# Performance work log

Hardware: AMD Instinct MI355X
Metric: run time of the kernel (lower is better)

The kernel has to match this reference:

```python
import jax, jax.numpy as jnp
import numpy as np

B, ORG, L = 128, 4, 2048
C1, C2 = 128, 64
K0, K1, K2 = 7, 5, 3
VQD, VQN = 64, 1024
CARD, NG = 32, 8
EPS = 1e-5


def _conv(x, w, groups=1):
    # 1D conv, stride 1, 'same' padding (k-1)//2, NCH layout, weight (O, I/g, K)
    p = (w.shape[-1] - 1) // 2
    return jax.lax.conv_general_dilated(
        x, w, (1,), [(p, p)],
        dimension_numbers=('NCH', 'OIH', 'NCH'), feature_group_count=groups)


def _tconv(x, w):
    # ConvTranspose1d(stride=1, padding=(k-1)//2) == conv with channel-transposed, spatially flipped kernel
    return _conv(x, jnp.flip(jnp.transpose(w, (1, 0, 2)), -1))


def _gn(x, g, b, groups=NG):
    Bx, C, T = x.shape
    xr = x.reshape(Bx, groups, C // groups, T)
    mu = xr.mean((2, 3), keepdims=True)
    var = xr.var((2, 3), keepdims=True)
    xn = ((xr - mu) * jax.lax.rsqrt(var + EPS)).reshape(Bx, C, T)
    return xn * g[None, :, None] + b[None, :, None]


def setup_inputs() -> dict:
    key = jax.random.key(0)
    ks = iter(jax.random.split(key, 32))
    w = lambda *s: jax.random.normal(next(ks), s, jnp.float32) * 0.05
    ones = lambda n: jnp.ones((n,), jnp.float32)
    zeros = lambda n: jnp.zeros((n,), jnp.float32)
    D = C1 // 2  # ResNeXt bottleneck width
    return dict(
        x=jax.random.normal(next(ks), (B, ORG, L), jnp.float32),
        w0=w(C1, ORG, K0), g0_g=ones(C1), g0_b=zeros(C1),
        wxa=w(D, C1, 1), gxa_g=ones(D), gxa_b=zeros(D),
        wxb=w(D, D // CARD, K1), gxb_g=ones(D), gxb_b=zeros(D),
        wxc=w(C1, D, 1), gxc_g=ones(C1), gxc_b=zeros(C1),
        w2=w(C2, C1, K2), bn2_g=ones(C2), bn2_b=zeros(C2),
        embed_w=jax.random.uniform(next(ks), (VQN, VQD), jnp.float32, -1.0 / VQD, 1.0 / VQD),
        wd2=w(C2, C1, K2), gd2_g=ones(C1), gd2_b=zeros(C1),
        wd1a=w(C1, C1, K1), gd1a_g=ones(C1), gd1a_b=zeros(C1),
        wd1b=w(C1, C1, K1), gd1b_g=ones(C1), gd1b_b=zeros(C1),
        wd0=w(C1, ORG, K0), bd0=zeros(ORG),
    )


def reference(x, w0, g0_g, g0_b, wxa, gxa_g, gxa_b, wxb, gxb_g, gxb_b,
              wxc, gxc_g, gxc_b, w2, bn2_g, bn2_b, embed_w,
              wd2, gd2_g, gd2_b, wd1a, gd1a_g, gd1a_b, wd1b, gd1b_g, gd1b_b,
              wd0, bd0):
    selu = jax.nn.selu

    # ---- encoder ----
    h = selu(_gn(_conv(x, w0), g0_g, g0_b))  # res0

    def resx(h):  # ResNeXt bottleneck, shared weights (module reuses self.resx)
        y = selu(_gn(_conv(h, wxa), gxa_g, gxa_b))
        y = selu(_gn(_conv(y, wxb, groups=CARD), gxb_g, gxb_b))
        y = _gn(_conv(y, wxc), gxc_g, gxc_b)
        return selu(h + y)

    pool = lambda t: t.reshape(t.shape[0], t.shape[1], -1, 2).max(-1)  # MaxPool1d(2)
    h = pool(resx(h))
    h = pool(resx(h))
    # res2: conv + BatchNorm (eval mode, running stats 0/1 -> affine)
    h = _conv(h, w2) * bn2_g[None, :, None] + bn2_b[None, :, None]

    # ---- vector quantization (vqc=True: quantize channel vectors) ----
    Bh, C, T = h.shape  # C == VQD
    Z = jnp.transpose(h, (0, 2, 1)).reshape(-1, VQD)  # [N, vq_dim]
    d = (jnp.sum(Z * Z, 1, keepdims=True) - 2.0 * (Z @ embed_w.T)
         + jnp.sum(embed_w * embed_w, 1)[None, :])  # [N, vq_num] squared L2
    j = jnp.argmin(d, axis=1)
    W_j = embed_w[j]
    commit_loss = jnp.mean(jnp.sum((Z - jax.lax.stop_gradient(W_j)) ** 2, -1))
    vq_loss = jnp.mean(jnp.sum((jax.lax.stop_gradient(Z) - W_j) ** 2, -1))
    hq = jnp.transpose(W_j.reshape(Bh, T, C), (0, 2, 1))  # back to [B, C, T]

    # ---- decoder ----
    up = lambda t: jnp.repeat(t, 2, axis=-1)  # nearest Upsample(x2)

    def deres1(h):  # basic residual block, shared weights (module reuses self.deres1)
        y = selu(_gn(_tconv(h, wd1a), gd1a_g, gd1a_b))
        y = _gn(_tconv(y, wd1b), gd1b_g, gd1b_b)
        return selu(h + y)

    h = selu(_gn(_tconv(hq, wd2), gd2_g, gd2_b))  # deres2
    h = deres1(up(h))
    h = deres1(up(h))
    recon = _tconv(h, wd0) + bd0[None, :, None]  # deres0 (with bias)
    return recon, commit_loss, vq_loss
```

## Files before the change

kernel.cpp:

```cpp
#include <hip/hip_runtime.h>
#include <math.h>

static constexpr int B_   = 128;
static constexpr int ORG_ = 4;
static constexpr int L_   = 2048;
static constexpr int C1_  = 128;
static constexpr int C2_  = 64;
static constexpr int NG_  = 8;
static constexpr int VQD_ = 64;
static constexpr int VQN_ = 1024;
static constexpr long PTS_ = (long)B_ * (L_ / 4);

typedef __attribute__((ext_vector_type(8))) short bf16x8;
typedef __attribute__((ext_vector_type(4))) float f32x4;

__device__ __forceinline__ float selu_f(float x) {
    const float scale = 1.0507009873554805f;
    const float alpha = 1.6732632423543772f;
    return scale * (x > 0.f ? x : alpha * expm1f(x));
}
__device__ __forceinline__ unsigned short f2bf(float x) {
    unsigned u = __float_as_uint(x);
    u = (u + 0x7FFFu + ((u >> 16) & 1u)) >> 16;
    return (unsigned short)u;
}
__device__ __forceinline__ float bf2f(unsigned short u) {
    return __uint_as_float((unsigned)u << 16);
}

__global__ void wprep_kernel(const float* __restrict__ w, float* __restrict__ wT,
                             int CO, int cig, int K, int so, int si, int sk, int koff)
{
    int idx = blockIdx.x * 256 + threadIdx.x;
    int total = cig * K * CO;
    if (idx >= total) return;
    int o = idx % CO;
    int r = idx / CO;
    int i = r / K, k = r % K;
    wT[idx] = w[(long)o * so + (long)i * si + (long)k * sk + koff];
}

__global__ void wprep_mfma_kernel(const float* __restrict__ w, unsigned short* __restrict__ wb)
{
    int idx = blockIdx.x * 256 + threadIdx.x;
    if (idx >= 5 * 16 * 128 * 8) return;
    int j  = idx & 7;
    int o  = (idx >> 3) & 127;
    int kk = idx >> 10;
    int ig = kk & 3, ic = (kk >> 2) & 3, k = kk >> 4;
    int i  = ic * 32 + ig * 8 + j;
    wb[idx] = f2bf(w[(long)i * (128 * 5) + o * 5 + (4 - k)]);
}

__global__ void fill_kernel(float* p, float v, int n)
{
    int i = blockIdx.x * 256 + threadIdx.x;
    if (i < n) p[i] = v;
}

template<int K, int CO, int NTHR, int TT, int OT, int VQ>
__global__ __launch_bounds__(NTHR) void conv_tile_kernel(
    const float* __restrict__ in, const float* __restrict__ wT,
    const float* __restrict__ scale, const float* __restrict__ bias,
    float* __restrict__ out,
    int CI, int T, int cig, int cog,
    const float* __restrict__ ist, const float* __restrict__ ig,
    const float* __restrict__ ibt, int icpg, int iselu,
    const float* __restrict__ res,
    float* __restrict__ vbest, int* __restrict__ vbj, int jbase, long vstride)
{
    constexpr int P    = (K - 1) / 2;
    constexpr int SPAN = TT + K - 1;
    constexpr int RS   = (SPAN + 3) & ~3;
    constexpr int NO   = CO / OT;
    constexpr int NT   = (CO * TT) / (NTHR * OT);
    constexpr int XW   = NT + K - 1;
    extern __shared__ float lds[];

    if constexpr (VQ) {
        const int z = blockIdx.z;
        wT    += (long)z * cig * K * CO;
        bias  += (long)z * CO;
        vbest += (long)z * vstride;
        vbj   += (long)z * vstride;
        jbase += z * CO;
    }

    const int tile = blockIdx.x;
    const int b    = blockIdx.y;
    const int t0g  = tile * TT;
    const float* inb = in + (long)b * CI * T;

    for (int idx = threadIdx.x; idx < CI * SPAN; idx += NTHR) {
        int c = idx / SPAN, j = idx % SPAN;
        int tt = t0g + j - P;
        float v = 0.f;
        if (tt >= 0 && tt < T) {
            v = inb[(long)c * T + tt];
            if (ist) {
                const float* s = &ist[2 * (b * NG_ + c / icpg)];
                v = (v - s[0]) * s[1] * ig[c] + ibt[c];
                if (res) v += res[((long)b * CI + c) * T + tt];
                if (iselu) v = selu_f(v);
            }
        }
        lds[c * RS + j] = v;
    }
    __syncthreads();

    const int o0   = (threadIdx.x % NO) * OT;
    const int slot = threadIdx.x / NO;
    const int t0   = slot * NT;
    const int g    = o0 / cog;
    const float* wrow = wT + o0;

    float acc[OT][NT];
#pragma unroll
    for (int oo = 0; oo < OT; ++oo)
#pragma unroll
        for (int u = 0; u < NT; ++u) acc[oo][u] = 0.f;

#pragma unroll 4
    for (int i = 0; i < cig; ++i) {
        const int irow = g * cig + i;
        float xin[(XW + 3) & ~3];
        if constexpr (NT % 4 == 0) {
            constexpr int X4 = (XW + 3) / 4;
            const float4* l4 = reinterpret_cast<const float4*>(&lds[irow * RS + t0]);
#pragma unroll
            for (int j = 0; j < X4; ++j) {
                float4 v = l4[j];
                xin[4 * j]     = v.x;
                xin[4 * j + 1] = v.y;
                xin[4 * j + 2] = v.z;
                xin[4 * j + 3] = v.w;
            }
        } else {
#pragma unroll
            for (int j = 0; j < XW; ++j) xin[j] = lds[irow * RS + t0 + j];
        }
        float wk[OT][K];
#pragma unroll
        for (int oo = 0; oo < OT; ++oo)
#pragma unroll
            for (int k = 0; k < K; ++k) wk[oo][k] = wrow[(i * K + k) * CO + oo];
#pragma unroll
        for (int oo = 0; oo < OT; ++oo)
#pragma unroll
            for (int u = 0; u < NT; ++u)
#pragma unroll
                for (int k = 0; k < K; ++k)
                    acc[oo][u] = fmaf(xin[u + k], wk[oo][k], acc[oo][u]);
    }

    if constexpr (VQ) {
        constexpr int RW = (NO >= 64) ? 64 : 32;
        const int lane = threadIdx.x & 63;
#pragma unroll
        for (int u = 0; u < NT; ++u) {
            float bv = 3.4e38f;
            int bj = 0;
#pragma unroll
            for (int oo = 0; oo < OT; ++oo) {
                const int o = o0 + oo;
                float sv = fmaf(acc[oo][u], scale[o], bias[o]);
                if (sv < bv) { bv = sv; bj = jbase + o; }
            }
#pragma unroll
            for (int off = 1; off < RW; off <<= 1) {
                float v2 = __shfl_xor(bv, off);
                int   j2 = __shfl_xor(bj, off);
                if (v2 < bv || (v2 == bv && j2 < bj)) { bv = v2; bj = j2; }
            }
            if ((lane & (RW - 1)) == 0) {
                long n = (long)b * T + t0g + t0 + u;
                vbest[n] = bv;
                vbj[n]   = bj;
            }
        }
    } else {
#pragma unroll
        for (int oo = 0; oo < OT; ++oo) {
            const int o = o0 + oo;
            const float sc = scale ? scale[o] : 1.f;
            const float bi = bias  ? bias[o]  : 0.f;
            float* ob = out + ((long)b * CO + o) * T + t0g + t0;
#pragma unroll
            for (int u = 0; u < NT; ++u) ob[u] = acc[oo][u] * sc + bi;
        }
    }
}

__global__ __launch_bounds__(256) void conv_epi7_kernel(
    const unsigned short* __restrict__ in, const float* __restrict__ wT,
    float* __restrict__ pbuf, int T, int Bc,
    const float* __restrict__ ist, const float* __restrict__ ig_,
    const float* __restrict__ ibt, int icpg,
    const unsigned short* __restrict__ res)
{
    __shared__ float wlds[32 * 7 * 4];
    __shared__ float rows[4][80];

    const int z   = blockIdx.z;
    const int ci0 = z * 32;

    for (int idx = threadIdx.x; idx < 32 * 7 * 4; idx += 256)
        wlds[idx] = wT[ci0 * 7 * 4 + idx];
    __syncthreads();

    const int wid  = threadIdx.x >> 6;
    const int lane = threadIdx.x & 63;
    const int b    = blockIdx.y;
    const int t0w  = blockIdx.x * 256 + wid * 64;
    const int t    = t0w + lane;
    float* row = rows[wid];
    const long base = (long)b * 128 * T;

    float acc0 = 0.f, acc1 = 0.f, acc2 = 0.f, acc3 = 0.f;

    for (int cc = 0; cc < 32; ++cc) {
        const int ci = ci0 + cc;
        const float* s = &ist[2 * (b * NG_ + ci / icpg)];
        const float mu = s[0], rs = s[1];
        const float gc = ig_[ci], bc = ibt[ci];
        const long cbase = base + (long)ci * T;

        float v = bf2f(in[cbase + t]);
        v = (v - mu) * rs * gc + bc;
        v += bf2f(res[cbase + t]);
        v = selu_f(v);
        row[3 + lane] = v;

        if (lane < 3 || lane >= 61) {
            int th   = (lane < 3) ? (t0w - 3 + lane) : (t0w + 3 + lane);
            int ridx = (lane < 3) ? lane : (lane + 6);
            float h = 0.f;
            if (th >= 0 && th < T) {
                h = bf2f(in[cbase + th]);
                h = (h - mu) * rs * gc + bc;
                h += bf2f(res[cbase + th]);
                h = selu_f(h);
            }
            row[ridx] = h;
        }

        float xin[7];
#pragma unroll
        for (int j = 0; j < 7; ++j) xin[j] = row[lane + j];
#pragma unroll
        for (int k = 0; k < 7; ++k) {
            float4 w4 = *(const float4*)&wlds[(cc * 7 + k) * 4];
            acc0 = fmaf(xin[k], w4.x, acc0);
            acc1 = fmaf(xin[k], w4.y, acc1);
            acc2 = fmaf(xin[k], w4.z, acc2);
            acc3 = fmaf(xin[k], w4.w, acc3);
        }
    }

    const long half = (long)Bc * 4 * T;
    float* pb = pbuf + (long)z * half + ((long)b * 4) * T + t;
    pb[0 * T] = acc0;
    pb[1 * T] = acc1;
    pb[2 * T] = acc2;
    pb[3 * T] = acc3;
}

__global__ void epi_comb_kernel(const float* __restrict__ pbuf,
                                const float* __restrict__ bias,
                                float* __restrict__ out, int T, int Bc, long total)
{
    const long half = (long)Bc * 4 * T;
    for (long idx = blockIdx.x * (long)blockDim.x + threadIdx.x; idx < total;
         idx += (long)gridDim.x * blockDim.x) {
        const int o = (int)((idx / T) & 3);
        float v = ((pbuf[idx] + pbuf[half + idx]) + pbuf[2 * half + idx])
                  + pbuf[3 * half + idx];
        out[idx] = v + bias[o];
    }
}

__global__ __launch_bounds__(256) void conv_mfma5_kernel(
    const unsigned short* __restrict__ in, const unsigned short* __restrict__ wb,
    unsigned short* __restrict__ out, int T,
    const float* __restrict__ ist, const float* __restrict__ ig_,
    const float* __restrict__ ibt, int icpg)
{
    constexpr int SPAN = 68, RSI = 136;
    __shared__ unsigned short xlds[SPAN * RSI];

    const int t0g = blockIdx.x * 64;
    const int b   = blockIdx.y;
    const unsigned short* inb = in + (long)b * 128 * T;

    for (int idx = threadIdx.x; idx < 128 * SPAN; idx += 256) {
        int i = idx / SPAN, j = idx % SPAN;
        int tt = t0g + j - 2;
        unsigned short raw = 0;
        if (tt >= 0 && tt < T) {
            raw = inb[(long)i * T + tt];
            if (ist) {
                const float* s = &ist[2 * (b * NG_ + i / icpg)];
                float v = selu_f((bf2f(raw) - s[0]) * s[1] * ig_[i] + ibt[i]);
                raw = f2bf(v);
            }
        }
        xlds[j * RSI + i] = raw;
    }
    __syncthreads();

    const int lane = threadIdx.x & 63;
    const int wid  = threadIdx.x >> 6;
    const int mr   = lane & 15;
    const int kg   = lane >> 4;

    f32x4 acc[4][2];
#pragma unroll
    for (int m = 0; m < 4; ++m)
#pragma unroll
        for (int oo = 0; oo < 2; ++oo) acc[m][oo] = (f32x4){0.f, 0.f, 0.f, 0.f};

#pragma unroll
    for (int k = 0; k < 5; ++k) {
#pragma unroll
        for (int ic = 0; ic < 4; ++ic) {
            bf16x8 a[4];
#pragma unroll
            for (int m = 0; m < 4; ++m)
                a[m] = *(const bf16x8*)&xlds[(m * 16 + mr + k) * RSI + ic * 32 + kg * 8];
            const unsigned short* wp = wb + (((k * 16 + ic * 4 + kg) * 128) + mr) * 8;
#pragma unroll
            for (int oo = 0; oo < 2; ++oo) {
                const int ot = wid * 2 + oo;
                bf16x8 bfr = *(const bf16x8*)(wp + ot * 16 * 8);
#pragma unroll
                for (int m = 0; m < 4; ++m)
                    acc[m][oo] = __builtin_amdgcn_mfma_f32_16x16x32_bf16(a[m], bfr, acc[m][oo], 0, 0, 0);
            }
        }
    }

#pragma unroll
    for (int m = 0; m < 4; ++m) {
#pragma unroll
        for (int oo = 0; oo < 2; ++oo) {
            const int ot = wid * 2 + oo;
            int o = ot * 16 + mr;
            ushort4 v;
            v.x = f2bf(acc[m][oo][0]);
            v.y = f2bf(acc[m][oo][1]);
            v.z = f2bf(acc[m][oo][2]);
            v.w = f2bf(acc[m][oo][3]);
            *(ushort4*)&out[((long)b * 128 + o) * T + t0g + m * 16 + kg * 4] = v;
        }
    }
}

__global__ __launch_bounds__(256) void gn_stats_kernel(
    const float* __restrict__ x, float* __restrict__ stats,
    int C, int T, int G)
{
    const int bg = blockIdx.x;
    const int cpg = C / G;
    const int b = bg / G, g = bg % G;
    const float* base = x + ((long)b * C + (long)g * cpg) * T;
    const long n4 = (long)cpg * T / 4;
    const float4* b4 = (const float4*)base;
    float s = 0.f, ss = 0.f;
    for (long i = threadIdx.x; i < n4; i += blockDim.x) {
        float4 v = b4[i];
        s += v.x + v.y + v.z + v.w;
        ss += v.x * v.x + v.y * v.y + v.z * v.z + v.w * v.w;
    }
#pragma unroll
    for (int off = 32; off; off >>= 1) {
        s  += __shfl_down(s, off);
        ss += __shfl_down(ss, off);
    }
    __shared__ float sh_s[4], sh_ss[4];
    const int wid = threadIdx.x >> 6, lane = threadIdx.x & 63;
    if (lane == 0) { sh_s[wid] = s; sh_ss[wid] = ss; }
    __syncthreads();
    if (threadIdx.x == 0) {
        float S = 0.f, SS = 0.f;
        for (int i = 0; i < 4; ++i) { S += sh_s[i]; SS += sh_ss[i]; }
        float inv_n = 1.f / (float)((long)cpg * T);
        float mu  = S * inv_n;
        float var = SS * inv_n - mu * mu;
        stats[2 * bg]     = mu;
        stats[2 * bg + 1] = rsqrtf(var + 1e-5f);
    }
}

__global__ __launch_bounds__(256) void gn_stats_bf16_kernel(
    const unsigned short* __restrict__ x, float* __restrict__ stats,
    int C, int T, int G)
{
    const int bg = blockIdx.x;
    const int cpg = C / G;
    const int b = bg / G, g = bg % G;
    const unsigned short* base = x + ((long)b * C + (long)g * cpg) * T;
    const long n8 = (long)cpg * T / 8;
    const uint4* b8 = (const uint4*)base;
    float s = 0.f, ss = 0.f;
    for (long i = threadIdx.x; i < n8; i += blockDim.x) {
        uint4 v = b8[i];
        unsigned ws[4] = {v.x, v.y, v.z, v.w};
#pragma unroll
        for (int q = 0; q < 4; ++q) {
            float f0 = __uint_as_float(ws[q] << 16);
            float f1 = __uint_as_float(ws[q] & 0xFFFF0000u);
            s += f0 + f1;
            ss += f0 * f0 + f1 * f1;
        }
    }
#pragma unroll
    for (int off = 32; off; off >>= 1) {
        s  += __shfl_down(s, off);
        ss += __shfl_down(ss, off);
    }
    __shared__ float sh_s[4], sh_ss[4];
    const int wid = threadIdx.x >> 6, lane = threadIdx.x & 63;
    if (lane == 0) { sh_s[wid] = s; sh_ss[wid] = ss; }
    __syncthreads();
    if (threadIdx.x == 0) {
        float S = 0.f, SS = 0.f;
        for (int i = 0; i < 4; ++i) { S += sh_s[i]; SS += sh_ss[i]; }
        float inv_n = 1.f / (float)((long)cpg * T);
        float mu  = S * inv_n;
        float var = SS * inv_n - mu * mu;
        stats[2 * bg]     = mu;
        stats[2 * bg + 1] = rsqrtf(var + 1e-5f);
    }
}

__global__ __launch_bounds__(256) void pool_fused_kernel(
    const float* __restrict__ x, const float* __restrict__ xst,
    const float* __restrict__ xg, const float* __restrict__ xb, int xcpg,
    const float* __restrict__ r, const float* __restrict__ rst,
    const float* __restrict__ rg, const float* __restrict__ rb, int rcpg, int rselu,
    float* __restrict__ out, int C, int Tout, long total)
{
    for (long idx = blockIdx.x * (long)blockDim.x + threadIdx.x; idx < total;
         idx += (long)gridDim.x * blockDim.x) {
        const int to = (int)(idx % Tout);
        const int c  = (int)((idx / Tout) % C);
        const int b  = (int)(idx / ((long)Tout * C));
        const long base = ((long)b * C + c) * (2 * Tout);
        const float* sx = &xst[2 * (b * NG_ + c / xcpg)];
        const float xgc = sx[1] * xg[c], xbc = xb[c] - sx[0] * sx[1] * xg[c];
        float rgc = 1.f, rbc = 0.f;
        if (rst) {
            const float* sr = &rst[2 * (b * NG_ + c / rcpg)];
            rgc = sr[1] * rg[c]; rbc = rb[c] - sr[0] * sr[1] * rg[c];
        }
        float f[2];
#pragma unroll
        for (int q = 0; q < 2; ++q) {
            long t = base + 2 * to + q;
            float rv = r[t] * rgc + rbc;
            if (rst && rselu) rv = selu_f(rv);
            f[q] = selu_f(x[t] * xgc + xbc + rv);
        }
        out[((long)b * C + c) * Tout + to] = fmaxf(f[0], f[1]);
    }
}

template<int INBF>
__global__ __launch_bounds__(256) void up_fused_kernel(
    const void* __restrict__ x_, const float* __restrict__ xst,
    const float* __restrict__ xg, const float* __restrict__ xb, int xcpg,
    const unsigned short* __restrict__ res,
    unsigned short* __restrict__ out, int C, int Tin, long total)
{
    for (long idx = blockIdx.x * (long)blockDim.x + threadIdx.x; idx < total;
         idx += (long)gridDim.x * blockDim.x) {
        const int t = (int)(idx % Tin);
        const int c = (int)((idx / Tin) % C);
        const int b = (int)(idx / ((long)Tin * C));
        const float* s = &xst[2 * (b * NG_ + c / xcpg)];
        float v = INBF ? bf2f(((const unsigned short*)x_)[idx])
                       : ((const float*)x_)[idx];
        v = (v - s[0]) * s[1] * xg[c] + xb[c];
        if (res) v += bf2f(res[idx]);
        v = selu_f(v);
        unsigned short h = f2bf(v);
        unsigned pack = (unsigned)h | ((unsigned)h << 16);
        *(unsigned*)(out + (((long)b * C + c) * Tin + t) * 2) = pack;
    }
}

__global__ void wnorm_kernel(const float* __restrict__ codes, float* __restrict__ wn)
{
    int j = blockIdx.x * 256 + threadIdx.x;
    if (j >= VQN_) return;
    const float* c = codes + (long)j * VQD_;
    float s = 0.f;
#pragma unroll
    for (int i = 0; i < VQD_; ++i) s = fmaf(c[i], c[i], s);
    wn[j] = s;
}

__global__ void vq_combine_kernel(const float* __restrict__ vb, const int* __restrict__ vj,
                                  int* __restrict__ bjs, long stride, int NP)
{
    int n = blockIdx.x * 256 + threadIdx.x;
    if (n >= NP) return;
    float best = vb[n];
    int bj = vj[n];
#pragma unroll
    for (int s = 1; s < 4; ++s) {
        float v = vb[(long)s * stride + n];
        if (v < best) { best = v; bj = vj[(long)s * stride + n]; }
    }
    bjs[n] = bj;
}

__global__ __launch_bounds__(256) void vq_gather_kernel(
    const float* __restrict__ h, const float* __restrict__ codes,
    const int* __restrict__ bjs, float* __restrict__ hq, float* __restrict__ loss,
    int T)
{
    const int n0 = blockIdx.x * 64;
    const int b  = n0 / T;
    const int tb = n0 % T;
    __shared__ int sbj[64];
    if (threadIdx.x < 64) sbj[threadIdx.x] = bjs[n0 + threadIdx.x];
    __syncthreads();

    float l = 0.f;
#pragma unroll
    for (int r = 0; r < (VQD_ * 64) / 256; ++r) {
        int idx = r * 256 + (int)threadIdx.x;
        int c  = idx >> 6, tl = idx & 63;
        float wv = codes[(long)sbj[tl] * VQD_ + c];
        long off = ((long)b * VQD_ + c) * T + tb + tl;
        hq[off] = wv;
        float df = h[off] - wv;
        l = fmaf(df, df, l);
    }
#pragma unroll
    for (int off = 32; off; off >>= 1) l += __shfl_down(l, off);
    if ((threadIdx.x & 63) == 0) atomicAdd(loss, l);
}

__global__ void zero_kernel(float* p) { p[0] = 0.f; }

__global__ void finalize_kernel(const float* __restrict__ loss, float* __restrict__ out,
                                float invNP, long off)
{
    float v = loss[0] * invNP;
    out[off]     = v;
    out[off + 1] = v;
}

static inline int nblk(long total, int thr = 256, long cap = 262144) {
    long b = (total + thr - 1) / thr;
    if (b > cap) b = cap;
    if (b < 1) b = 1;
    return (int)b;
}
static inline int ldsz(int CI, int K, int TT = 64) {
    int span = TT + K - 1;
    int rs = (span + 3) & ~3;
    return CI * rs * 4;
}

struct WT {
    long w0, wxa, wxb, wxc, w2, wd2, wd0, total;
};
static WT wt_offsets() {
    WT o; long p = 0;
    o.w0   = p; p += (long)ORG_ * 7 * C1_;
    o.wxa  = p; p += (long)C1_ * 1 * (C1_ / 2);
    o.wxb  = p; p += 2L * 5 * (C1_ / 2);
    o.wxc  = p; p += (long)(C1_ / 2) * 1 * C1_;
    o.w2   = p; p += (long)C1_ * 3 * C2_;
    o.wd2  = p; p += (long)C2_ * 3 * C1_;
    o.wd0  = p; p += (long)C1_ * 7 * ORG_;
    o.total = p;
    return o;
}

static void run_chunk(const float* x, const float* const* W, const float* wt,
                      const WT& wo, const unsigned short* wbA, const unsigned short* wbB,
                      const float* wn, const float* wts, const float* neg2,
                      float* vbest4, int* vbj4, int* bjs, float* out,
                      float* A, float* Bb, float* Cc, float* st, float* lossbuf,
                      int Bc, long nbuf, hipStream_t stream)
{
    const float* g0_g  = W[1];
    const float* g0_b  = W[2];
    const float* gxa_g = W[4];
    const float* gxa_b = W[5];
    const float* gxb_g = W[7];
    const float* gxb_b = W[8];
    const float* gxc_g = W[10];
    const float* gxc_b = W[11];
    const float* bn2_g = W[13];
    const float* bn2_b = W[14];
    const float* embed = W[15];
    const float* gd2_g = W[17];
    const float* gd2_b = W[18];
    const float* gd1a_g= W[20];
    const float* gd1a_b= W[21];
    const float* gd1b_g= W[23];
    const float* gd1b_b= W[24];
    const float* bd0   = W[26];

    const int D_ = C1_ / 2;
    const int SLOT = 2048;
    float* st0 = st + 0 * SLOT;
    float* st1 = st + 1 * SLOT;
    float* st2 = st + 2 * SLOT;
    float* st3 = st + 3 * SLOT;
    float* st4 = st + 4 * SLOT;
    float* st5 = st + 5 * SLOT;
    float* st6 = st + 6 * SLOT;

    unsigned short* Au  = (unsigned short*)A;
    unsigned short* Bbu = (unsigned short*)Bb;
    unsigned short* Ccu = (unsigned short*)Cc;

    const int nbg = Bc * NG_;
    const int cpg1 = C1_ / NG_;

    int T = L_;

    conv_tile_kernel<7, 128, 512, 64, 1, 0><<<dim3(T / 64, Bc), 512, ldsz(ORG_, 7), stream>>>(
        x, wt + wo.w0, nullptr, nullptr, A, ORG_, T, ORG_, C1_,
        nullptr, nullptr, nullptr, 0, 0, nullptr, nullptr, nullptr, 0, 0);
    gn_stats_kernel<<<nbg, 256, 0, stream>>>(A, st0, C1_, T, NG_);

    conv_tile_kernel<1, 64, 512, 64, 2, 0><<<dim3(T / 64, Bc), 512, ldsz(C1_, 1), stream>>>(
        A, wt + wo.wxa, nullptr, nullptr, Bb, C1_, T, C1_, D_,
        st0, g0_g, g0_b, cpg1, 1, nullptr, nullptr, nullptr, 0, 0);
    gn_stats_kernel<<<nbg, 256, 0, stream>>>(Bb, st1, D_, T, NG_);

    conv_tile_kernel<5, 64, 512, 64, 1, 0><<<dim3(T / 64, Bc), 512, ldsz(D_, 5), stream>>>(
        Bb, wt + wo.wxb, nullptr, nullptr, Bb + nbuf / 2, D_, T, 2, 2,
        st1, gxa_g, gxa_b, D_ / NG_, 1, nullptr, nullptr, nullptr, 0, 0);
    gn_stats_kernel<<<nbg, 256, 0, stream>>>(Bb + nbuf / 2, st2, D_, T, NG_);

    conv_tile_kernel<1, 128, 512, 64, 2, 0><<<dim3(T / 64, Bc), 512, ldsz(D_, 1), stream>>>(
        Bb + nbuf / 2, wt + wo.wxc, nullptr, nullptr, Cc, D_, T, D_, C1_,
        st2, gxb_g, gxb_b, D_ / NG_, 1, nullptr, nullptr, nullptr, 0, 0);
    gn_stats_kernel<<<nbg, 256, 0, stream>>>(Cc, st3, C1_, T, NG_);

    {
        int Tout = T / 2;
        long tt = (long)Bc * C1_ * Tout;
        pool_fused_kernel<<<nblk(tt), 256, 0, stream>>>(
            Cc, st3, gxc_g, gxc_b, cpg1,
            A, st0, g0_g, g0_b, cpg1, 1,
            Bb, C1_, Tout, tt);
        T = Tout;
    }

    conv_tile_kernel<1, 64, 512, 64, 2, 0><<<dim3(T / 64, Bc), 512, ldsz(C1_, 1), stream>>>(
        Bb, wt + wo.wxa, nullptr, nullptr, Cc, C1_, T, C1_, D_,
        nullptr, nullptr, nullptr, 0, 0, nullptr, nullptr, nullptr, 0, 0);
    gn_stats_kernel<<<nbg, 256, 0, stream>>>(Cc, st1, D_, T, NG_);

    conv_tile_kernel<5, 64, 512, 64, 1, 0><<<dim3(T / 64, Bc), 512, ldsz(D_, 5), stream>>>(
        Cc, wt + wo.wxb, nullptr, nullptr, Cc + nbuf / 2, D_, T, 2, 2,
        st1, gxa_g, gxa_b, D_ / NG_, 1, nullptr, nullptr, nullptr, 0, 0);
    gn_stats_kernel<<<nbg, 256, 0, stream>>>(Cc + nbuf / 2, st2, D_, T, NG_);

    conv_tile_kernel<1, 128, 512, 64, 2, 0><<<dim3(T / 64, Bc), 512, ldsz(D_, 1), stream>>>(
        Cc + nbuf / 2, wt + wo.wxc, nullptr, nullptr, A, D_, T, D_, C1_,
        st2, gxb_g, gxb_b, D_ / NG_, 1, nullptr, nullptr, nullptr, 0, 0);
    gn_stats_kernel<<<nbg, 256, 0, stream>>>(A, st3, C1_, T, NG_);

    {
        int Tout = T / 2;
        long tt = (long)Bc * C1_ * Tout;
        pool_fused_kernel<<<nblk(tt), 256, 0, stream>>>(
            A, st3, gxc_g, gxc_b, cpg1,
            Bb, nullptr, nullptr, nullptr, 0, 0,
            Cc, C1_, Tout, tt);
        T = Tout;
    }

    conv_tile_kernel<3, 64, 512, 64, 1, 0><<<dim3(T / 64, Bc), 512, ldsz(C1_, 3), stream>>>(
        Cc, wt + wo.w2, bn2_g, bn2_b, Bb, C1_, T, C1_, C2_,
        nullptr, nullptr, nullptr, 0, 0, nullptr, nullptr, nullptr, 0, 0);

    {
        int NP = Bc * T;
        conv_tile_kernel<1, 256, 512, 64, 8, 1><<<dim3(T / 64, Bc, 4), 512,
                                                  ldsz(VQD_, 1), stream>>>(
            Bb, wts, neg2, wn, nullptr,
            VQD_, T, VQD_, 256,
            nullptr, nullptr, nullptr, 0, 0, nullptr,
            vbest4, vbj4, 0, PTS_);
        vq_combine_kernel<<<(NP + 255) / 256, 256, 0, stream>>>(vbest4, vbj4, bjs, PTS_, NP);
        vq_gather_kernel<<<NP / 64, 256, 0, stream>>>(Bb, embed, bjs, A, lossbuf, T);
    }

    conv_tile_kernel<3, 128, 512, 64, 1, 0><<<dim3(T / 64, Bc), 512, ldsz(C2_, 3), stream>>>(
        A, wt + wo.wd2, nullptr, nullptr, Bb, C2_, T, C2_, C1_,
        nullptr, nullptr, nullptr, 0, 0, nullptr, nullptr, nullptr, 0, 0);
    gn_stats_kernel<<<nbg, 256, 0, stream>>>(Bb, st4, C1_, T, NG_);

    {
        long tt = (long)Bc * C1_ * T;
        up_fused_kernel<0><<<nblk(tt), 256, 0, stream>>>(
            Bb, st4, gd2_g, gd2_b, cpg1, nullptr, Ccu, C1_, T, tt);
        T *= 2;
    }

    conv_mfma5_kernel<<<dim3(T / 64, Bc), 256, 0, stream>>>(
        Ccu, wbA, Au, T, nullptr, nullptr, nullptr, 0);
    gn_stats_bf16_kernel<<<nbg, 256, 0, stream>>>(Au, st5, C1_, T, NG_);

    conv_mfma5_kernel<<<dim3(T / 64, Bc), 256, 0, stream>>>(
        Au, wbB, Bbu, T, st5, gd1a_g, gd1a_b, cpg1);
    gn_stats_bf16_kernel<<<nbg, 256, 0, stream>>>(Bbu, st6, C1_, T, NG_);

    {
        long tt = (long)Bc * C1_ * T;
        up_fused_kernel<1><<<nblk(tt), 256, 0, stream>>>(
            Bbu, st6, gd1b_g, gd1b_b, cpg1, Ccu, Au, C1_, T, tt);
        T *= 2;
    }

    conv_mfma5_kernel<<<dim3(T / 64, Bc), 256, 0, stream>>>(
        Au, wbA, Ccu, T, nullptr, nullptr, nullptr, 0);
    gn_stats_bf16_kernel<<<nbg, 256, 0, stream>>>(Ccu, st5, C1_, T, NG_);

    conv_mfma5_kernel<<<dim3(T / 64, Bc), 256, 0, stream>>>(
        Ccu, wbB, Bbu, T, st5, gd1a_g, gd1a_b, cpg1);
    gn_stats_bf16_kernel<<<nbg, 256, 0, stream>>>(Bbu, st6, C1_, T, NG_);

    {
        float* pbuf = Cc;
        conv_epi7_kernel<<<dim3(T / 256, Bc, 4), 256, 0, stream>>>(
            Bbu, wt + wo.wd0, pbuf, T, Bc,
            st6, gd1b_g, gd1b_b, cpg1, Au);
        long tt = (long)Bc * 4 * T;
        epi_comb_kernel<<<nblk(tt), 256, 0, stream>>>(pbuf, bd0, out, T, Bc, tt);
    }
}

extern "C" void kernel_launch(void* const* d_in, const int* in_sizes, int n_in,
                              void* d_out, int out_size, void* d_ws, size_t ws_size,
                              hipStream_t stream) {
    const float* x = (const float*)d_in[0];
    const float* W[27];
    for (int i = 0; i < 27; ++i) W[i] = (const float*)d_in[i + 1];

    float* out = (float*)d_out;
    const WT wo = wt_offsets();

    const long WT_F32  = 262144;
    const long WB_F32  = 2 * 81920 / 2;
    const long WTS_F32 = VQN_ * VQD_;
    const long ST_F32  = 8 * 2048;
    const long VQ_F32  = 4 * PTS_ + 4 * PTS_ + PTS_;
    const long FIXED = WT_F32 + WB_F32 + 1024 + WTS_F32 + 256 + ST_F32 + 64 + VQ_F32;
    int Bc = 0;
    for (int cand = B_; cand >= 1; cand >>= 1) {
        size_t need = ((size_t)FIXED + (size_t)3 * cand * C1_ * L_) * sizeof(float);
        if (need <= ws_size) { Bc = cand; break; }
    }
    if (Bc == 0) return;

    float* wt            = (float*)d_ws;
    unsigned short* wbA  = (unsigned short*)(wt + WT_F32);
    unsigned short* wbB  = wbA + 81920;
    float* wn            = wt + WT_F32 + WB_F32;
    float* wts           = wn + 1024;
    float* neg2          = wts + WTS_F32;
    float* st            = neg2 + 256;
    float* lossbuf       = st + ST_F32;
    float* vbest4        = lossbuf + 64;
    int*   vbj4          = (int*)(vbest4 + 4 * PTS_);
    int*   bjs           = vbj4 + 4 * PTS_;
    const long nbuf = (long)Bc * C1_ * L_;
    float* A  = (float*)(bjs + PTS_);
    float* Bb = A + nbuf;
    float* Cc = Bb + nbuf;

    const int D_ = C1_ / 2;

    auto prep = [&](const float* w, long off, int CO, int cig, int K,
                    int so, int si, int sk, int koff) {
        int total = cig * K * CO;
        wprep_kernel<<<(total + 255) / 256, 256, 0, stream>>>(
            w, wt + off, CO, cig, K, so, si, sk, koff);
    };
    prep(W[0],  wo.w0,   C1_, ORG_, 7, ORG_ * 7, 7,        1,  0);
    prep(W[3],  wo.wxa,  D_,  C1_,  1, C1_,      1,        1,  0);
    prep(W[6],  wo.wxb,  D_,  2,    5, 2 * 5,    5,        1,  0);
    prep(W[9],  wo.wxc,  C1_, D_,   1, D_,       1,        1,  0);
    prep(W[12], wo.w2,   C2_, C1_,  3, C1_ * 3,  3,        1,  0);
    prep(W[16], wo.wd2,  C1_, C2_,  3, 3,        C1_ * 3, -1,  2);
    prep(W[25], wo.wd0,  ORG_, C1_, 7, 7,        ORG_ * 7, -1, 6);
    wprep_mfma_kernel<<<81920 / 256, 256, 0, stream>>>(W[19], wbA);
    wprep_mfma_kernel<<<81920 / 256, 256, 0, stream>>>(W[22], wbB);
    wnorm_kernel<<<(VQN_ + 255) / 256, 256, 0, stream>>>(W[15], wn);
    for (int q = 0; q < 4; ++q) {
        wprep_kernel<<<(256 * VQD_ + 255) / 256, 256, 0, stream>>>(
            W[15] + (long)q * 256 * VQD_, wts + (long)q * 256 * VQD_,
            256, VQD_, 1, VQD_, 1, 1, 0);
    }
    fill_kernel<<<1, 256, 0, stream>>>(neg2, -2.f, 256);

    zero_kernel<<<1, 1, 0, stream>>>(lossbuf);

    for (int b0 = 0; b0 < B_; b0 += Bc) {
        const float* xc = x + (long)b0 * ORG_ * L_;
        float* outc = out + (long)b0 * ORG_ * L_;
        run_chunk(xc, W, wt, wo, wbA, wbB, wn, wts, neg2, vbest4, vbj4, bjs,
                  outc, A, Bb, Cc, st, lossbuf, Bc, nbuf, stream);
    }

    {
        float invNP = 1.f / (float)(B_ * (L_ / 4));
        finalize_kernel<<<1, 1, 0, stream>>>(lossbuf, out, invNP, (long)out_size - 2);
    }
}
```

Baseline: 2.022 ms.

## Fuse GroupNorm statistics into the MFMA conv epilogue via atomics

The 5-tap bf16 MFMA conv kernel now reduces per-group sum and sum-of-squares from its fp32 accumulators. It adds them into a zeroed workspace buffer with atomicAdd, and a tiny finalize kernel turns them into mean and rstd. This replaces the four gn_stats_bf16 passes, which re-read the large upsampled decoder activations from memory. The trade-offs are atomic contention across time tiles, an extra zeroing launch, and stats taken from unrounded fp32 values instead of the stored bf16 output.

```diff
diff --git a/kernel.cpp b/kernel.cpp
--- a/kernel.cpp
+++ b/kernel.cpp
@@ -56,6 +56,24 @@
 {
     int i = blockIdx.x * 256 + threadIdx.x;
     if (i < n) p[i] = v;
+}
+
+__global__ void zero_n_kernel(float* p, int n)
+{
+    int i = blockIdx.x * 256 + threadIdx.x;
+    if (i < n) p[i] = 0.f;
+}
+
+__global__ void gnfin_kernel(const float* __restrict__ raw, float* __restrict__ st,
+                             float invn, int n)
+{
+    int i = blockIdx.x * 64 + threadIdx.x;
+    if (i >= n) return;
+    float s = raw[2 * i], ss = raw[2 * i + 1];
+    float mu = s * invn;
+    float var = ss * invn - mu * mu;
+    st[2 * i] = mu;
+    st[2 * i + 1] = rsqrtf(var + 1e-5f);
 }
 
 template<int K, int CO, int NTHR, int TT, int OT, int VQ>
@@ -283,7 +301,8 @@
     const unsigned short* __restrict__ in, const unsigned short* __restrict__ wb,
     unsigned short* __restrict__ out, int T,
     const float* __restrict__ ist, const float* __restrict__ ig_,
-    const float* __restrict__ ibt, int icpg)
+    const float* __restrict__ ibt, int icpg,
+    float* __restrict__ ostat)
 {
     constexpr int SPAN = 68, RSI = 136;
     __shared__ unsigned short xlds[SPAN * RSI];
@@ -351,6 +370,30 @@
             v.z = f2bf(acc[m][oo][2]);
             v.w = f2bf(acc[m][oo][3]);
             *(ushort4*)&out[((long)b * 128 + o) * T + t0g + m * 16 + kg * 4] = v;
+        }
+    }
+
+    if (ostat) {
+#pragma unroll
+        for (int oo = 0; oo < 2; ++oo) {
+            float s = 0.f, ss = 0.f;
+#pragma unroll
+            for (int m = 0; m < 4; ++m)
+#pragma unroll
+                for (int q = 0; q < 4; ++q) {
+                    float v = acc[m][oo][q];
+                    s += v; ss = fmaf(v, v, ss);
+                }
+#pragma unroll
+            for (int off = 32; off; off >>= 1) {
+                s  += __shfl_down(s, off);
+                ss += __shfl_down(ss, off);
+            }
+            if (lane == 0) {
+                const int grp = wid * 2 + oo;
+                atomicAdd(&ostat[2 * (b * NG_ + grp)],     s);
+                atomicAdd(&ostat[2 * (b * NG_ + grp) + 1], ss);
+            }
         }
     }
 }
@@ -370,48 +413,6 @@
         float4 v = b4[i];
         s += v.x + v.y + v.z + v.w;
         ss += v.x * v.x + v.y * v.y + v.z * v.z + v.w * v.w;
-    }
-#pragma unroll
-    for (int off = 32; off; off >>= 1) {
-        s  += __shfl_down(s, off);
-        ss += __shfl_down(ss, off);
-    }
-    __shared__ float sh_s[4], sh_ss[4];
-    const int wid = threadIdx.x >> 6, lane = threadIdx.x & 63;
-    if (lane == 0) { sh_s[wid] = s; sh_ss[wid] = ss; }
-    __syncthreads();
-    if (threadIdx.x == 0) {
-        float S = 0.f, SS = 0.f;
-        for (int i = 0; i < 4; ++i) { S += sh_s[i]; SS += sh_ss[i]; }
-        float inv_n = 1.f / (float)((long)cpg * T);
-        float mu  = S * inv_n;
-        float var = SS * inv_n - mu * mu;
-        stats[2 * bg]     = mu;
-        stats[2 * bg + 1] = rsqrtf(var + 1e-5f);
-    }
-}
-
-__global__ __launch_bounds__(256) void gn_stats_bf16_kernel(
-    const unsigned short* __restrict__ x, float* __restrict__ stats,
-    int C, int T, int G)
-{
-    const int bg = blockIdx.x;
-    const int cpg = C / G;
-    const int b = bg / G, g = bg % G;
-    const unsigned short* base = x + ((long)b * C + (long)g * cpg) * T;
-    const long n8 = (long)cpg * T / 8;
-    const uint4* b8 = (const uint4*)base;
-    float s = 0.f, ss = 0.f;
-    for (long i = threadIdx.x; i < n8; i += blockDim.x) {
-        uint4 v = b8[i];
-        unsigned ws[4] = {v.x, v.y, v.z, v.w};
-#pragma unroll
-        for (int q = 0; q < 4; ++q) {
-            float f0 = __uint_as_float(ws[q] << 16);
-            float f1 = __uint_as_float(ws[q] & 0xFFFF0000u);
-            s += f0 + f1;
-            ss += f0 * f0 + f1 * f1;
-        }
     }
 #pragma unroll
     for (int off = 32; off; off >>= 1) {
@@ -616,6 +617,7 @@
     float* st4 = st + 4 * SLOT;
     float* st5 = st + 5 * SLOT;
     float* st6 = st + 6 * SLOT;
+    float* stR = st + 8 * SLOT;
 
     unsigned short* Au  = (unsigned short*)A;
     unsigned short* Bbu = (unsigned short*)Bb;
@@ -625,6 +627,8 @@
     const int cpg1 = C1_ / NG_;
 
     int T = L_;
+
+    zero_n_kernel<<<(4 * SLOT + 255) / 256, 256, 0, stream>>>(stR, 4 * SLOT);
 
     conv_tile_kernel<7, 128, 512, 64, 1, 0><<<dim3(T / 64, Bc), 512, ldsz(ORG_, 7), stream>>>(
         x, wt + wo.w0, nullptr, nullptr, A, ORG_, T, ORG_, C1_,
@@ -710,12 +714,12 @@
     }
 
     conv_mfma5_kernel<<<dim3(T / 64, Bc), 256, 0, stream>>>(
-        Ccu, wbA, Au, T, nullptr, nullptr, nullptr, 0);
-    gn_stats_bf16_kernel<<<nbg, 256, 0, stream>>>(Au, st5, C1_, T, NG_);
+        Ccu, wbA, Au, T, nullptr, nullptr, nullptr, 0, stR + 0 * SLOT);
+    gnfin_kernel<<<(nbg + 63) / 64, 64, 0, stream>>>(stR + 0 * SLOT, st5, 1.f / (16.f * T), nbg);
 
     conv_mfma5_kernel<<<dim3(T / 64, Bc), 256, 0, stream>>>(
-        Au, wbB, Bbu, T, st5, gd1a_g, gd1a_b, cpg1);
-    gn_stats_bf16_kernel<<<nbg, 256, 0, stream>>>(Bbu, st6, C1_, T, NG_);
+        Au, wbB, Bbu, T, st5, gd1a_g, gd1a_b, cpg1, stR + 1 * SLOT);
+    gnfin_kernel<<<(nbg + 63) / 64, 64, 0, stream>>>(stR + 1 * SLOT, st6, 1.f / (16.f * T), nbg);
 
     {
         long tt = (long)Bc * C1_ * T;
@@ -725,12 +729,12 @@
     }
 
     conv_mfma5_kernel<<<dim3(T / 64, Bc), 256, 0, stream>>>(
-        Au, wbA, Ccu, T, nullptr, nullptr, nullptr, 0);
-    gn_stats_bf16_kernel<<<nbg, 256, 0, stream>>>(Ccu, st5, C1_, T, NG_);
+        Au, wbA, Ccu, T, nullptr, nullptr, nullptr, 0, stR + 2 * SLOT);
+    gnfin_kernel<<<(nbg + 63) / 64, 64, 0, stream>>>(stR + 2 * SLOT, st5, 1.f / (16.f * T), nbg);
 
     conv_mfma5_kernel<<<dim3(T / 64, Bc), 256, 0, stream>>>(
-        Ccu, wbB, Bbu, T, st5, gd1a_g, gd1a_b, cpg1);
-    gn_stats_bf16_kernel<<<nbg, 256, 0, stream>>>(Bbu, st6, C1_, T, NG_);
+        Ccu, wbB, Bbu, T, st5, gd1a_g, gd1a_b, cpg1, stR + 3 * SLOT);
+    gnfin_kernel<<<(nbg + 63) / 64, 64, 0, stream>>>(stR + 3 * SLOT, st6, 1.f / (16.f * T), nbg);
 
     {
         float* pbuf = Cc;
@@ -755,7 +759,7 @@
     const long WT_F32  = 262144;
     const long WB_F32  = 2 * 81920 / 2;
     const long WTS_F32 = VQN_ * VQD_;
-    const long ST_F32  = 8 * 2048;
+    const long ST_F32  = 12 * 2048;
     const long VQ_F32  = 4 * PTS_ + 4 * PTS_ + PTS_;
     const long FIXED = WT_F32 + WB_F32 + 1024 + WTS_F32 + 256 + ST_F32 + 64 + VQ_F32;
     int Bc = 0;
```

After: 1.973 ms (median of 2 runs). 1.02x faster.
